# Kernel tuning notes

Measured on AMD Instinct MI355X. Metric: run time of the kernel, lower is better.

Reference implementation:

```python
import jax, jax.numpy as jnp
import numpy as np

LAYERS = 2      # LightGCN propagation layers
LAMB = 0.5      # aux loss weight
REG = 1e-4      # embedding reg weight
N_AUX = 2       # len(behaviors) - 1


def setup_inputs() -> dict:
    key = jax.random.key(0)
    k = jax.random.split(key, 8)
    n_users, n_items, d = 100000, 50000, 32
    E = 1000000
    user_emb = (jax.random.normal(k[0], (n_users + 1, d), jnp.float32) * 0.1).at[0].set(0.0)
    item_emb = (jax.random.normal(k[1], (n_items + 1, d), jnp.float32) * 0.1).at[0].set(0.0)
    aux_u = jax.random.randint(k[2], (N_AUX, E), 1, n_users + 1)
    aux_i = jax.random.randint(k[3], (N_AUX, E), 1, n_items + 1)
    aux_edges = jnp.stack([aux_u, aux_i], axis=-1).astype(jnp.int32)
    tgt_u = jax.random.randint(k[4], (E,), 1, n_users + 1)
    tgt_i = jax.random.randint(k[5], (E,), 1, n_items + 1)
    target_edges = jnp.stack([tgt_u, tgt_i], axis=-1).astype(jnp.int32)
    # [B, 1+N_AUX, 3]: per row (user, pos_item, neg_item) for target then each aux behavior
    batch_data = jax.random.randint(k[6], (4096, 1 + N_AUX, 3), 1, n_items + 1).astype(jnp.int32)
    return {"user_emb": user_emb, "item_emb": item_emb, "batch_data": batch_data,
            "aux_edges": aux_edges, "target_edges": target_edges}


def _graph(edges, n_user_rows, N):
    """Symmetric-normalized bipartite LightGCN graph as directed COO (src, dst, w)."""
    u = edges[:, 0]
    v = edges[:, 1] + n_user_rows  # shift item ids into joint node space
    ones = jnp.ones(u.shape[0], jnp.float32)
    deg = jax.ops.segment_sum(ones, u, num_segments=N) + jax.ops.segment_sum(ones, v, num_segments=N)
    dinv = jnp.where(deg > 0, jax.lax.rsqrt(jnp.maximum(deg, 1.0)), 0.0)
    w = dinv[u] * dinv[v]
    src = jnp.concatenate([u, v])
    dst = jnp.concatenate([v, u])
    w2 = jnp.concatenate([w, w])
    return src, dst, w2


def _lightgcn(emb, src, dst, w, N):
    """L-layer LightGCN propagation, mean over layers 0..L."""
    acc = emb
    cur = emb
    for _ in range(LAYERS):
        cur = jax.ops.segment_sum(w[:, None] * cur[src], dst, num_segments=N)
        acc = acc + cur
    return acc / (LAYERS + 1)


def _prob(ue, ie, u, i):
    return jax.nn.relu(jnp.sum(ue[u] * ie[i], axis=-1))


def _bpr(p, n):
    return -jnp.mean(jax.nn.log_sigmoid(p - n))


def reference(user_emb, item_emb, batch_data, aux_edges, target_edges):
    Nu = user_emb.shape[0]
    N = Nu + item_emb.shape[0]
    all_emb = jnp.concatenate([user_emb, item_emb], axis=0)
    tgt_g = _graph(target_edges, Nu, N)

    user, p_item, n_item = batch_data[:, 0, 0], batch_data[:, 0, 1], batch_data[:, 0, 2]
    aux_user, aux_p, aux_n = batch_data[:, 1:, 0], batch_data[:, 1:, 1], batch_data[:, 1:, 2]

    cps, cns, dps, dns, aps, ans, aux_losses = [], [], [], [], [], [], []
    for idx in range(N_AUX):
        # combine graph = aux behavior edges union target edges
        comb_edges = jnp.concatenate([aux_edges[idx], target_edges], axis=0)
        ce = _lightgcn(all_emb, *_graph(comb_edges, Nu, N), N)
        cu, ci = ce[:Nu], ce[Nu:]
        cps.append(_prob(cu, ci, user, p_item))
        cns.append(_prob(cu, ci, user, n_item))

        ae = _lightgcn(all_emb, *_graph(aux_edges[idx], Nu, N), N)
        au, ai = ae[:Nu], ae[Nu:]
        aps.append(_prob(au, ai, user, p_item))
        ans.append(_prob(au, ai, user, n_item))

        # condition: propagate aux embeddings through the target graph
        de = _lightgcn(ae, *tgt_g, N)
        du, di = de[:Nu], de[Nu:]
        dps.append(_prob(du, di, user, p_item))
        dns.append(_prob(du, di, user, n_item))

        ps = jnp.sum(au[aux_user[:, idx]] * ai[aux_p[:, idx]], axis=-1)
        ns = jnp.sum(au[aux_user[:, idx]] * ai[aux_n[:, idx]], axis=-1)
        aux_losses.append(_bpr(ps, ns))

    aux_loss = jnp.mean(jnp.stack(aux_losses))

    def front_door(cond, comb, aux):
        return jnp.sum(cond * jnp.sum(comb * aux, axis=0), axis=0)

    p_scores = front_door(jnp.stack(dps), jnp.stack(cps), jnp.stack(aps))
    n_scores = front_door(jnp.stack(dns), jnp.stack(cns), jnp.stack(ans))
    rec_loss = _bpr(p_scores, n_scores)
    emb_loss = (jnp.linalg.norm(user_emb) + jnp.linalg.norm(item_emb)) / item_emb.shape[0]
    return rec_loss + LAMB * aux_loss + REG * emb_loss
```

## Files before the change

kernel.cpp:

```cpp
#include <hip/hip_runtime.h>
#include <hip/hip_fp16.h>
#include <math.h>

#define D 32
#define ROWU 16
#define NBK 1024
#define BSHIFT 8
#define TILE_H 16384
#define TILE_BIN 2048

typedef unsigned int u32;
typedef unsigned short u16;

__device__ __forceinline__ float logsigf(float x) {
  return fminf(x, 0.f) - log1pf(expf(-fabsf(x)));
}

__device__ __forceinline__ float lo16(u32 u) { return __uint_as_float(u << 16); }
__device__ __forceinline__ float hi16(u32 u) { return __uint_as_float(u & 0xFFFF0000u); }
__device__ __forceinline__ u32 pk2(float a, float b) {
  u32 ua = __float_as_uint(a), ub = __float_as_uint(b);
  u32 ra = (ua + 0x7FFFu + ((ua >> 16) & 1u)) >> 16;
  u32 rb = (ub + 0x7FFFu + ((ub >> 16) & 1u)) >> 16;
  return (ra & 0xFFFFu) | (rb << 16);
}
__device__ __forceinline__ float bfat(const u16* __restrict__ p, size_t off) {
  return __uint_as_float(((u32)p[off]) << 16);
}
__device__ __forceinline__ void accum8(float* a, float w, uint4 x) {
  a[0] += w * lo16(x.x); a[1] += w * hi16(x.x);
  a[2] += w * lo16(x.y); a[3] += w * hi16(x.y);
  a[4] += w * lo16(x.z); a[5] += w * hi16(x.z);
  a[6] += w * lo16(x.w); a[7] += w * hi16(x.w);
}
__device__ __forceinline__ uint4 pack8(const float* a, float w) {
  return make_uint4(pk2(w * a[0], w * a[1]), pk2(w * a[2], w * a[3]),
                    pk2(w * a[4], w * a[5]), pk2(w * a[6], w * a[7]));
}

__device__ __forceinline__ u32 wpack(float a, float b) {
  __half2 h = __floats2half2_rn(a, b);
  return *reinterpret_cast<u32*>(&h);
}
__device__ __forceinline__ float2 hun(int wb) {
  __half2 h;
  *reinterpret_cast<int*>(&h) = wb;
  return __half22float2(h);
}


__global__ void hist_kernel(const int2* __restrict__ tgt, const int2* __restrict__ aux,
                            int E, int Nu, int BPS, int* __restrict__ bcur) {
  __shared__ int lh[NBK];
  int seg = blockIdx.x / BPS;
  int blk = blockIdx.x - seg * BPS;
  const int2* edges = (seg == 0) ? tgt : aux + (size_t)(seg - 1) * E;
  for (int b = threadIdx.x; b < NBK; b += 256) lh[b] = 0;
  __syncthreads();
  int e0 = blk * TILE_H;
  for (int k = threadIdx.x; k < TILE_H; k += 256) {
    int e = e0 + k;
    if (e < E) {
      int2 ed = edges[e];
      atomicAdd(&lh[ed.x >> BSHIFT], 1);
      atomicAdd(&lh[(ed.y + Nu) >> BSHIFT], 1);
    }
  }
  __syncthreads();
  for (int b = threadIdx.x; b < NBK; b += 256)
    if (lh[b]) atomicAdd(&bcur[seg * NBK + b], lh[b]);
}

__global__ void bscan_kernel(int* __restrict__ bcur) {
  int* b = bcur + blockIdx.x * NBK;
  int lane = threadIdx.x;
  int carry = 0;
  for (int base = 0; base < NBK; base += 64) {
    int i = base + lane;
    int v = b[i];
    int s = v;
    #pragma unroll
    for (int o = 1; o < 64; o <<= 1) {
      int t = __shfl_up(s, o);
      if (lane >= o) s += t;
    }
    b[i] = carry + s - v;
    carry += __shfl(s, 63);
  }
}

__global__ void bin_kernel(const int2* __restrict__ tgt, const int2* __restrict__ aux,
                           int E, int Nu, int BPS, int* __restrict__ bcur,
                           int* __restrict__ binned) {
  __shared__ int stage[2 * TILE_BIN];
  __shared__ u16 stagebk[2 * TILE_BIN];
  __shared__ int lh[NBK];
  __shared__ int loff[NBK];
  __shared__ int gb[NBK];
  __shared__ int wred[4];
  __shared__ int stot;
  int seg = blockIdx.x / BPS;
  int blk = blockIdx.x - seg * BPS;
  const int2* edges = (seg == 0) ? tgt : aux + (size_t)(seg - 1) * E;
  int* out = binned + (size_t)seg * 2 * E;
  int tid = threadIdx.x;
  for (int b = tid; b < NBK; b += 256) lh[b] = 0;
  __syncthreads();
  int e0 = blk * TILE_BIN;
  int pkv[16];
  int pb[16];
  int pr[16];
  #pragma unroll
  for (int it = 0; it < 8; ++it) {
    int e = e0 + tid + it * 256;
    bool ok = e < E;
    int2 ed = ok ? edges[e] : make_int2(0, -Nu);
    int u = ed.x, v = ed.y + Nu;
    int b1 = u >> BSHIFT, b2 = v >> BSHIFT;
    pkv[2 * it] = ((u & 255) << 18) | v;
    pb[2 * it] = b1;
    pr[2 * it] = ok ? atomicAdd(&lh[b1], 1) : 0;
    pkv[2 * it + 1] = ((v & 255) << 18) | u;
    pb[2 * it + 1] = b2;
    pr[2 * it + 1] = ok ? atomicAdd(&lh[b2], 1) : 0;
  }
  __syncthreads();
  int lane = tid & 63, wid = tid >> 6;
  int b4 = tid * 4;
  int v0 = lh[b4], v1 = lh[b4 + 1], v2 = lh[b4 + 2], v3 = lh[b4 + 3];
  int tsum = v0 + v1 + v2 + v3;
  int incl = tsum;
  #pragma unroll
  for (int o = 1; o < 64; o <<= 1) {
    int t = __shfl_up(incl, o);
    if (lane >= o) incl += t;
  }
  if (lane == 63) wred[wid] = incl;
  __syncthreads();
  int wbase = 0;
  for (int w = 0; w < wid; ++w) wbase += wred[w];
  int excl = wbase + incl - tsum;
  loff[b4] = excl;
  loff[b4 + 1] = excl + v0;
  loff[b4 + 2] = excl + v0 + v1;
  loff[b4 + 3] = excl + v0 + v1 + v2;
  if (tid == 255) stot = excl + tsum;
  #pragma unroll
  for (int j = 0; j < 4; ++j) {
    int b = b4 + j;
    int c = lh[b];
    gb[b] = c ? atomicAdd(&bcur[seg * NBK + b], c) : 0;
  }
  __syncthreads();
  #pragma unroll
  for (int it = 0; it < 16; ++it) {
    int e = e0 + tid + (it >> 1) * 256;
    if (e < E) {
      int pos = loff[pb[it]] + pr[it];
      stage[pos] = pkv[it];
      stagebk[pos] = (u16)pb[it];
    }
  }
  __syncthreads();
  int tot = stot;
  for (int k = tid; k < tot; k += 256) {
    int b = stagebk[k];
    out[gb[b] + (k - loff[b])] = stage[k];
  }
}

__global__ void csr_count_kernel(const int* __restrict__ binned,
                                 const int* __restrict__ bend, int E2, int N, int NBKe,
                                 int* __restrict__ deg3, int* __restrict__ rp3) {
  __shared__ int cnt[256];
  __shared__ int wred[4];
  int seg = blockIdx.x / NBKe;
  int bkt = blockIdx.x - seg * NBKe;
  int node0 = bkt << BSHIFT;
  const int* bc = bend + seg * NBK;
  int start = (bkt == 0) ? 0 : bc[bkt - 1];
  int end = bc[bkt];
  int cntE = end - start;
  const int* src = binned + (size_t)seg * E2 + start;
  cnt[threadIdx.x] = 0;
  __syncthreads();
  for (int k = threadIdx.x; k < cntE; k += 256) atomicAdd(&cnt[src[k] >> 18], 1);
  __syncthreads();
  int lane = threadIdx.x & 63, wid = threadIdx.x >> 6;
  int v = cnt[threadIdx.x];
  int incl = v;
  #pragma unroll
  for (int o = 1; o < 64; o <<= 1) {
    int t = __shfl_up(incl, o);
    if (lane >= o) incl += t;
  }
  if (lane == 63) wred[wid] = incl;
  __syncthreads();
  int wbase = 0;
  for (int w = 0; w < wid; ++w) wbase += wred[w];
  int node = node0 + (int)threadIdx.x;
  if (node < N) {
    deg3[(size_t)seg * N + node] = v;
    rp3[(size_t)seg * (N + 1) + node] = start + wbase + incl - v;
  }
  if (bkt == 0 && threadIdx.x == 0) rp3[(size_t)seg * (N + 1) + N] = E2;
}

__global__ void dinv_all_kernel(const int* __restrict__ deg3, float* __restrict__ dinv5,
                                u32* __restrict__ wtab, int N) {
  int n = blockIdx.x * blockDim.x + threadIdx.x;
  if (n >= N) return;
  int dt = deg3[n], d0 = deg3[N + n], d1 = deg3[2 * N + n];
  float wt  = dt ? rsqrtf((float)dt) : 0.f;
  float wa0 = d0 ? rsqrtf((float)d0) : 0.f;
  float wa1 = d1 ? rsqrtf((float)d1) : 0.f;
  int c0 = dt + d0, c1 = dt + d1;
  float wc0 = c0 ? rsqrtf((float)c0) : 0.f;
  float wc1 = c1 ? rsqrtf((float)c1) : 0.f;
  dinv5[n] = wt;
  dinv5[N + n] = wa0;
  dinv5[2 * N + n] = wa1;
  dinv5[3 * N + n] = wc0;
  dinv5[4 * N + n] = wc1;
  wtab[n] = wpack(wc0, wc1);
  wtab[N + n] = wpack(wa0, wc0);
  wtab[2 * N + n] = wpack(wa1, wc1);
}

__global__ void csr_scatter_kernel(const int* __restrict__ binned,
                                   const int* __restrict__ bend,
                                   const int* __restrict__ rp3,
                                   const u32* __restrict__ wtab,
                                   int E2, int N, int NBKe,
                                   int2* __restrict__ pk) {
  __shared__ int cnt[256];
  __shared__ int off[256];
  int seg = blockIdx.x / NBKe;
  int bkt = blockIdx.x - seg * NBKe;
  int node0 = bkt << BSHIFT;
  const int* bc = bend + seg * NBK;
  int start = (bkt == 0) ? 0 : bc[bkt - 1];
  int end = bc[bkt];
  int cntE = end - start;
  const int* src = binned + (size_t)seg * E2 + start;
  int node = node0 + (int)threadIdx.x;
  off[threadIdx.x] = (node < N) ? rp3[(size_t)seg * (N + 1) + node] : 0;
  cnt[threadIdx.x] = 0;
  const u32* wt = wtab + (size_t)seg * N;
  __syncthreads();
  int2* out = pk + (size_t)seg * E2;
  for (int k = threadIdx.x; k < cntE; k += 256) {
    int en = src[k];
    int lb = en >> 18;
    int c = en & 0x3FFFF;
    int pos = atomicAdd(&cnt[lb], 1);
    out[off[lb] + pos] = make_int2(c, (int)wt[c]);
  }
}

__global__ void cvt_emb_kernel(const float2* __restrict__ ue, long nu2,
                               const float2* __restrict__ ie, long ni2,
                               u32* __restrict__ emb) {
  long i = (long)blockIdx.x * blockDim.x + threadIdx.x;
  if (i >= nu2 + ni2) return;
  float2 v = (i < nu2) ? ue[i] : ie[i - nu2];
  emb[i] = pk2(v.x, v.y);
}


__device__ __forceinline__ void edge1_dual(const int2* __restrict__ p, int j, int lane,
                                           const uint4* __restrict__ rows,
                                           float* a1, float* a2) {
  int2 en = p[j];
  float2 w = hun(en.y);
  uint4 x = rows[(size_t)en.x * 4 + lane];
  accum8(a1, w.x, x);
  accum8(a2, w.y, x);
}

__device__ __forceinline__ void stream_dual(const int* __restrict__ rp,
                                            const int2* __restrict__ p, int n, int lane,
                                            const uint4* __restrict__ rows,
                                            float* a1, float* a2) {
  int j = rp[n], e = rp[n + 1];
  if ((j & 1) && j < e) { edge1_dual(p, j, lane, rows, a1, a2); ++j; }
  for (; j + 3 < e; j += 4) {
    int4 m0 = *reinterpret_cast<const int4*>(p + j);
    int4 m1 = *reinterpret_cast<const int4*>(p + j + 2);
    uint4 x0 = rows[(size_t)m0.x * 4 + lane];
    uint4 x1 = rows[(size_t)m0.z * 4 + lane];
    uint4 x2 = rows[(size_t)m1.x * 4 + lane];
    uint4 x3 = rows[(size_t)m1.z * 4 + lane];
    float2 w0 = hun(m0.y), w1 = hun(m0.w), w2 = hun(m1.y), w3 = hun(m1.w);
    accum8(a1, w0.x, x0); accum8(a2, w0.y, x0);
    accum8(a1, w1.x, x1); accum8(a2, w1.y, x1);
    accum8(a1, w2.x, x2); accum8(a2, w2.y, x2);
    accum8(a1, w3.x, x3); accum8(a2, w3.y, x3);
  }
  for (; j < e; ++j) edge1_dual(p, j, lane, rows, a1, a2);
}

__global__ void gather_fused_all_kernel(const int* __restrict__ rp3,
                                        const int2* __restrict__ pk,
                                        const float* __restrict__ dinv5,
                                        const uint4* __restrict__ emb,
                                        uint4* __restrict__ BaAll, uint4* __restrict__ BcAll,
                                        int N, int E2) {
  const int* rpA0 = rp3 + (size_t)(N + 1);
  const int* rpA1 = rp3 + 2 * (size_t)(N + 1);
  const int2* pT = pk;
  const int2* pA0 = pk + (size_t)E2;
  const int2* pA1 = pk + 2 * (size_t)E2;
  const float* dvA0 = dinv5 + (size_t)N;
  const float* dvA1 = dinv5 + 2 * (size_t)N;
  const float* dvC0 = dinv5 + 3 * (size_t)N;
  const float* dvC1 = dinv5 + 4 * (size_t)N;
  int t = blockIdx.x * blockDim.x + threadIdx.x;
  int n = t >> 2;
  if (n >= N) return;
  int lane = t & 3;
  float aA0[8] = {0, 0, 0, 0, 0, 0, 0, 0};
  float aA1[8] = {0, 0, 0, 0, 0, 0, 0, 0};
  float aC0[8] = {0, 0, 0, 0, 0, 0, 0, 0};
  float aC1[8] = {0, 0, 0, 0, 0, 0, 0, 0};
  stream_dual(rpA0, pA0, n, lane, emb, aA0, aC0);
  stream_dual(rpA1, pA1, n, lane, emb, aA1, aC1);
  stream_dual(rp3, pT, n, lane, emb, aC0, aC1);
  size_t o = (size_t)n * 4 + lane;
  size_t rowN4 = (size_t)N * 4;
  BaAll[o] = pack8(aA0, dvA0[n]);
  BaAll[rowN4 + o] = pack8(aA1, dvA1[n]);
  BcAll[o] = pack8(aC0, dvC0[n]);
  BcAll[rowN4 + o] = pack8(aC1, dvC1[n]);
}

__global__ void gather_avg_kernel(const int* __restrict__ rp3, const int2* __restrict__ pk,
                                  const float* __restrict__ dinv5,
                                  const uint4* __restrict__ emb,
                                  const uint4* __restrict__ BaAll, uint4* __restrict__ AI,
                                  int N, int E2) {
  int idx = blockIdx.y;
  const int* rp = rp3 + (size_t)(1 + idx) * (N + 1);
  const int2* pA = pk + (size_t)(1 + idx) * E2;
  const float* dv = dinv5 + (size_t)(1 + idx) * N;
  const uint4* cur = BaAll + (size_t)idx * N * 4;
  int t = blockIdx.x * blockDim.x + threadIdx.x;
  int n = t >> 2;
  if (n >= N) return;
  int lane = t & 3;
  float acc[8] = {0, 0, 0, 0, 0, 0, 0, 0};
  int j = rp[n], e = rp[n + 1];
  if ((j & 1) && j < e) {
    int2 en = pA[j];
    uint4 x = cur[(size_t)en.x * 4 + lane];
    accum8(acc, hun(en.y).x, x);
    ++j;
  }
  for (; j + 3 < e; j += 4) {
    int4 m0 = *reinterpret_cast<const int4*>(pA + j);
    int4 m1 = *reinterpret_cast<const int4*>(pA + j + 2);
    uint4 x0 = cur[(size_t)m0.x * 4 + lane];
    uint4 x1 = cur[(size_t)m0.z * 4 + lane];
    uint4 x2 = cur[(size_t)m1.x * 4 + lane];
    uint4 x3 = cur[(size_t)m1.z * 4 + lane];
    accum8(acc, hun(m0.y).x, x0);
    accum8(acc, hun(m0.w).x, x1);
    accum8(acc, hun(m1.y).x, x2);
    accum8(acc, hun(m1.w).x, x3);
  }
  for (; j < e; ++j) {
    int2 en = pA[j];
    uint4 x = cur[(size_t)en.x * 4 + lane];
    accum8(acc, hun(en.y).x, x);
  }
  float wn = dv[n];
  uint4 e4 = emb[(size_t)n * 4 + lane];
  uint4 b4 = cur[(size_t)n * 4 + lane];
  float r[8];
  r[0] = (lo16(e4.x) + lo16(b4.x) + wn * acc[0]) * (1.f / 3.f);
  r[1] = (hi16(e4.x) + hi16(b4.x) + wn * acc[1]) * (1.f / 3.f);
  r[2] = (lo16(e4.y) + lo16(b4.y) + wn * acc[2]) * (1.f / 3.f);
  r[3] = (hi16(e4.y) + hi16(b4.y) + wn * acc[3]) * (1.f / 3.f);
  r[4] = (lo16(e4.z) + lo16(b4.z) + wn * acc[4]) * (1.f / 3.f);
  r[5] = (hi16(e4.z) + hi16(b4.z) + wn * acc[5]) * (1.f / 3.f);
  r[6] = (lo16(e4.w) + lo16(b4.w) + wn * acc[6]) * (1.f / 3.f);
  r[7] = (hi16(e4.w) + hi16(b4.w) + wn * acc[7]) * (1.f / 3.f);
  AI[(size_t)n * 8 + idx * 4 + lane] = pack8(r, 1.f);
}

__global__ void de_gather_kernel(const int* __restrict__ rp3, const int2* __restrict__ pk,
                                 const float* __restrict__ dinv5,
                                 const uint4* __restrict__ AI, uint4* __restrict__ DeI,
                                 int N) {
  int t = blockIdx.x * blockDim.x + threadIdx.x;
  int n = t >> 3;
  if (n >= N) return;
  int lane = t & 7;
  float acc[8] = {0, 0, 0, 0, 0, 0, 0, 0};
  int j = rp3[n], e = rp3[n + 1];
  if ((j & 1) && j < e) {
    int c = pk[j].x;
    uint4 x = AI[(size_t)c * 8 + lane];
    accum8(acc, dinv5[c], x);
    ++j;
  }
  for (; j + 3 < e; j += 4) {
    int4 m0 = *reinterpret_cast<const int4*>(pk + j);
    int4 m1 = *reinterpret_cast<const int4*>(pk + j + 2);
    uint4 x0 = AI[(size_t)m0.x * 8 + lane];
    uint4 x1 = AI[(size_t)m0.z * 8 + lane];
    uint4 x2 = AI[(size_t)m1.x * 8 + lane];
    uint4 x3 = AI[(size_t)m1.z * 8 + lane];
    accum8(acc, dinv5[m0.x], x0);
    accum8(acc, dinv5[m0.z], x1);
    accum8(acc, dinv5[m1.x], x2);
    accum8(acc, dinv5[m1.z], x3);
  }
  for (; j < e; ++j) {
    int c = pk[j].x;
    uint4 x = AI[(size_t)c * 8 + lane];
    accum8(acc, dinv5[c], x);
  }
  DeI[(size_t)n * 8 + lane] = pack8(acc, dinv5[n]);
}


__device__ __forceinline__ float fdim2(const int2* __restrict__ pkA, const int2* __restrict__ pkT,
                                       const int* __restrict__ rpA, const int* __restrict__ rpT,
                                       int idx, const float* __restrict__ dv,
                                       const u16* __restrict__ base, const u16* __restrict__ L1,
                                       int r, int d) {
  float acc = 0.f;
  for (int j = rpA[r]; j < rpA[r + 1]; ++j) {
    int2 en = pkA[j];
    acc += hun(en.y).y * bfat(L1, (size_t)en.x * D + d);
  }
  for (int j = rpT[r]; j < rpT[r + 1]; ++j) {
    int2 en = pkT[j];
    float2 w = hun(en.y);
    acc += (idx ? w.y : w.x) * bfat(L1, (size_t)en.x * D + d);
  }
  return (bfat(base, (size_t)r * D + d) + bfat(L1, (size_t)r * D + d) + dv[r] * acc) * (1.f / 3.f);
}

__device__ __forceinline__ float fdim1i(const int2* __restrict__ pkT, const int* __restrict__ rp,
                                        const float* __restrict__ dv,
                                        const u16* __restrict__ base, const u16* __restrict__ L1,
                                        int r, int di) {
  float acc = 0.f;
  for (int j = rp[r]; j < rp[r + 1]; ++j) {
    int2 en = pkT[j];
    acc += dv[en.x] * bfat(L1, (size_t)en.x * 64 + di);
  }
  return (bfat(base, (size_t)r * 64 + di) + bfat(L1, (size_t)r * 64 + di) + dv[r] * acc) * (1.f / 3.f);
}

__global__ void ce_sparse_kernel(const int* __restrict__ rp3, const int2* __restrict__ pk,
                                 const float* __restrict__ dinv5,
                                 const u32* __restrict__ EMBu, const u32* __restrict__ BcAll,
                                 const int* __restrict__ batch, int Bsz, int Nu, int N, int E2,
                                 float* __restrict__ cps, float* __restrict__ cns) {
  int idx = blockIdx.y;
  const int* rpA = rp3 + (size_t)(1 + idx) * (N + 1);
  const int2* pkA = pk + (size_t)(1 + idx) * E2;
  const float* dv = dinv5 + (size_t)(3 + idx) * N;
  const u16* base = (const u16*)EMBu;
  const u16* L1 = (const u16*)(BcAll + (size_t)idx * N * ROWU);
  float* outp = cps + (size_t)idx * Bsz;
  float* outn = cns + (size_t)idx * Bsz;
  int t = blockIdx.x * blockDim.x + threadIdx.x;
  int b = t >> 5, d = t & 31;
  if (b >= Bsz) return;
  int u = batch[b * 9 + 0];
  int p = batch[b * 9 + 1] + Nu;
  int n = batch[b * 9 + 2] + Nu;
  float uv = fdim2(pkA, pk, rpA, rp3, idx, dv, base, L1, u, d);
  float pv = fdim2(pkA, pk, rpA, rp3, idx, dv, base, L1, p, d);
  float nv = fdim2(pkA, pk, rpA, rp3, idx, dv, base, L1, n, d);
  float sp = uv * pv, sn = uv * nv;
  #pragma unroll
  for (int o = 16; o > 0; o >>= 1) {
    sp += __shfl_down(sp, o, 32);
    sn += __shfl_down(sn, o, 32);
  }
  if (d == 0) {
    outp[b] = fmaxf(sp, 0.f);
    outn[b] = fmaxf(sn, 0.f);
  }
}

__global__ void de_sparse_kernel(const int* __restrict__ rp3, const int2* __restrict__ pk,
                                 const float* __restrict__ dinv5,
                                 const u32* __restrict__ AI, const u32* __restrict__ DeI,
                                 const int* __restrict__ batch, int Bsz, int Nu, int N,
                                 float* __restrict__ dps, float* __restrict__ dns) {
  int idx = blockIdx.y;
  const u16* base = (const u16*)AI;
  const u16* L1 = (const u16*)DeI;
  float* outp = dps + (size_t)idx * Bsz;
  float* outn = dns + (size_t)idx * Bsz;
  int t = blockIdx.x * blockDim.x + threadIdx.x;
  int b = t >> 5, d = t & 31;
  if (b >= Bsz) return;
  int di = idx * 32 + d;
  int u = batch[b * 9 + 0];
  int p = batch[b * 9 + 1] + Nu;
  int n = batch[b * 9 + 2] + Nu;
  float uv = fdim1i(pk, rp3, dinv5, base, L1, u, di);
  float pv = fdim1i(pk, rp3, dinv5, base, L1, p, di);
  float nv = fdim1i(pk, rp3, dinv5, base, L1, n, di);
  float sp = uv * pv, sn = uv * nv;
  #pragma unroll
  for (int o = 16; o > 0; o >>= 1) {
    sp += __shfl_down(sp, o, 32);
    sn += __shfl_down(sn, o, 32);
  }
  if (d == 0) {
    outp[b] = fmaxf(sp, 0.f);
    outn[b] = fmaxf(sn, 0.f);
  }
}


__device__ __forceinline__ float dotrow(const u32* __restrict__ a, const u32* __restrict__ b) {
  float s = 0.f;
  #pragma unroll
  for (int k = 0; k < ROWU; ++k) {
    u32 x = a[k], y = b[k];
    s += lo16(x) * lo16(y) + hi16(x) * hi16(y);
  }
  return s;
}

__global__ void score_aux_kernel(const u32* __restrict__ AI, const int* __restrict__ batch,
                                 int Bsz, int Nu, int N, float* __restrict__ aps,
                                 float* __restrict__ ans_, float* __restrict__ accs) {
  int idx = blockIdx.y;
  const u32* A = AI + (size_t)idx * ROWU;
  float* outp = aps + (size_t)idx * Bsz;
  float* outn = ans_ + (size_t)idx * Bsz;
  int b = blockIdx.x * blockDim.x + threadIdx.x;
  float l = 0.f;
  if (b < Bsz) {
    int u = batch[b * 9 + 0];
    int p = batch[b * 9 + 1] + Nu;
    int n = batch[b * 9 + 2] + Nu;
    const u32* ur = A + (size_t)u * 32;
    outp[b] = fmaxf(dotrow(ur, A + (size_t)p * 32), 0.f);
    outn[b] = fmaxf(dotrow(ur, A + (size_t)n * 32), 0.f);
    const int* r = batch + b * 9 + 3 * (1 + idx);
    const u32* aur = A + (size_t)r[0] * 32;
    float ps = dotrow(aur, A + (size_t)(r[1] + Nu) * 32);
    float ns = dotrow(aur, A + (size_t)(r[2] + Nu) * 32);
    l = -logsigf(ps - ns);
  }
  for (int o = 32; o > 0; o >>= 1) l += __shfl_down(l, o);
  if ((threadIdx.x & 63) == 0) atomicAdd(&accs[idx], l);
}

__global__ void recloss_kernel(const float* __restrict__ cps, const float* __restrict__ cns,
                               const float* __restrict__ aps, const float* __restrict__ ans_,
                               const float* __restrict__ dps, const float* __restrict__ dns,
                               int Bsz, int NA, float* __restrict__ acc) {
  int b = blockIdx.x * blockDim.x + threadIdx.x;
  float l = 0.f;
  if (b < Bsz) {
    float dp = 0.f, dn = 0.f, cap = 0.f, can = 0.f;
    for (int i = 0; i < NA; ++i) {
      dp += dps[i * Bsz + b];
      dn += dns[i * Bsz + b];
      cap += cps[i * Bsz + b] * aps[i * Bsz + b];
      can += cns[i * Bsz + b] * ans_[i * Bsz + b];
    }
    l = -logsigf(dp * cap - dn * can);
  }
  for (int o = 32; o > 0; o >>= 1) l += __shfl_down(l, o);
  if ((threadIdx.x & 63) == 0) atomicAdd(acc, l);
}

__global__ void sumsq2_kernel(const float4* __restrict__ xu, int n4u,
                              const float4* __restrict__ xi, int n4i,
                              float* __restrict__ accU, float* __restrict__ accI) {
  __shared__ float redU[4], redI[4];
  int tid = threadIdx.x;
  int gid = blockIdx.x * blockDim.x + tid;
  int stride = gridDim.x * blockDim.x;
  float su = 0.f, si = 0.f;
  for (int i = gid; i < n4u; i += stride) {
    float4 v = xu[i];
    su += v.x * v.x + v.y * v.y + v.z * v.z + v.w * v.w;
  }
  for (int i = gid; i < n4i; i += stride) {
    float4 v = xi[i];
    si += v.x * v.x + v.y * v.y + v.z * v.z + v.w * v.w;
  }
  for (int o = 32; o > 0; o >>= 1) {
    su += __shfl_down(su, o);
    si += __shfl_down(si, o);
  }
  if ((tid & 63) == 0) { redU[tid >> 6] = su; redI[tid >> 6] = si; }
  __syncthreads();
  if (tid == 0) {
    atomicAdd(accU, redU[0] + redU[1] + redU[2] + redU[3]);
    atomicAdd(accI, redI[0] + redI[1] + redI[2] + redI[3]);
  }
}

__global__ void final_kernel(const float* __restrict__ accs, int Bsz, int NA, int NiRows,
                             float* __restrict__ out) {
  float rec = accs[NA] / (float)Bsz;
  float aux = 0.f;
  for (int i = 0; i < NA; ++i) aux += accs[i] / (float)Bsz;
  aux /= (float)NA;
  float embl = (sqrtf(accs[NA + 1]) + sqrtf(accs[NA + 2])) / (float)NiRows;
  out[0] = rec + 0.5f * aux + 1e-4f * embl;
}

extern "C" void kernel_launch(void* const* d_in, const int* in_sizes, int n_in,
                              void* d_out, int out_size, void* d_ws, size_t ws_size,
                              hipStream_t stream) {
  const float* user_emb = (const float*)d_in[0];
  const float* item_emb = (const float*)d_in[1];
  const int* batch = (const int*)d_in[2];
  const int* aux_edges = (const int*)d_in[3];
  const int* tgt_edges = (const int*)d_in[4];

  const int NuRows = in_sizes[0] / D;
  const int NiRows = in_sizes[1] / D;
  const int Bsz = in_sizes[2] / 9;
  const int E = in_sizes[4] / 2;
  const int NA = in_sizes[3] / (2 * E);
  const int N = NuRows + NiRows;
  const int E2 = 2 * E;
  const size_t rowH = (size_t)N * ROWU;
  const int BPS_H = (E + TILE_H - 1) / TILE_H;
  const int BPS_B = (E + TILE_BIN - 1) / TILE_BIN;
  const int NBKe = (N + (1 << BSHIFT) - 1) >> BSHIFT;

  u32* EMBu = (u32*)d_ws;
  u32* AI = EMBu + rowH;
  u32* BaAll = AI + 2 * rowH;
  u32* BcAll = BaAll + 2 * rowH;
  int* deg3 = (int*)(BcAll + 2 * rowH);
  float* dinv5 = (float*)(deg3 + 3 * (size_t)N);
  u32* wtab = (u32*)(dinv5 + 5 * (size_t)N);
  int* rp3 = (int*)(wtab + 3 * (size_t)N);
  int* bcur = rp3 + 3 * (size_t)(N + 1);
  uintptr_t pka = ((uintptr_t)(bcur + 3 * (size_t)NBK) + 15) & ~(uintptr_t)15;
  int2* pk = (int2*)pka;
  float* cps = (float*)(pk + 3 * (size_t)E2);
  float* cns = cps + (size_t)NA * Bsz;
  float* aps = cns + (size_t)NA * Bsz;
  float* ans_ = aps + (size_t)NA * Bsz;
  float* dps = ans_ + (size_t)NA * Bsz;
  float* dns = dps + (size_t)NA * Bsz;
  float* accs = dns + (size_t)NA * Bsz;
  int* binned = (int*)AI;

  const int TB = 256;
  const int gN = (N + TB - 1) / TB;
  const int gN4 = (N * 4 + TB - 1) / TB;
  const int gN8 = (N * 8 + TB - 1) / TB;
  const int gB = (Bsz + TB - 1) / TB;
  const int gB32 = (Bsz * 32 + TB - 1) / TB;
  const long nu2 = (long)NuRows * ROWU;
  const long ni2 = (long)NiRows * ROWU;
  const int gCvt = (int)((nu2 + ni2 + TB - 1) / TB);

  cvt_emb_kernel<<<gCvt, TB, 0, stream>>>((const float2*)user_emb, nu2,
                                          (const float2*)item_emb, ni2, EMBu);

  hipMemsetAsync(bcur, 0, 3 * (size_t)NBK * sizeof(int), stream);
  hist_kernel<<<3 * BPS_H, TB, 0, stream>>>((const int2*)tgt_edges, (const int2*)aux_edges,
                                            E, NuRows, BPS_H, bcur);
  bscan_kernel<<<3, 64, 0, stream>>>(bcur);
  bin_kernel<<<3 * BPS_B, TB, 0, stream>>>((const int2*)tgt_edges, (const int2*)aux_edges,
                                           E, NuRows, BPS_B, bcur, binned);
  csr_count_kernel<<<3 * NBKe, TB, 0, stream>>>(binned, bcur, E2, N, NBKe, deg3, rp3);
  dinv_all_kernel<<<gN, TB, 0, stream>>>(deg3, dinv5, wtab, N);
  csr_scatter_kernel<<<3 * NBKe, TB, 0, stream>>>(binned, bcur, rp3, wtab, E2, N, NBKe, pk);

  hipMemsetAsync(accs, 0, (size_t)(NA + 3) * sizeof(float), stream);

  dim3 gridG(gN4, NA), gridB(gB, NA), gridS(gB32, NA);

  gather_fused_all_kernel<<<gN4, TB, 0, stream>>>(rp3, pk, dinv5, (const uint4*)EMBu,
                                                  (uint4*)BaAll, (uint4*)BcAll, N, E2);
  gather_avg_kernel<<<gridG, TB, 0, stream>>>(rp3, pk, dinv5, (const uint4*)EMBu,
                                              (const uint4*)BaAll, (uint4*)AI, N, E2);
  score_aux_kernel<<<gridB, TB, 0, stream>>>(AI, batch, Bsz, NuRows, N, aps, ans_, accs);
  ce_sparse_kernel<<<gridS, TB, 0, stream>>>(rp3, pk, dinv5, EMBu, BcAll,
                                             batch, Bsz, NuRows, N, E2, cps, cns);
  de_gather_kernel<<<gN8, TB, 0, stream>>>(rp3, pk, dinv5, (const uint4*)AI,
                                           (uint4*)BaAll, N);
  de_sparse_kernel<<<gridS, TB, 0, stream>>>(rp3, pk, dinv5, AI, (const u32*)BaAll,
                                             batch, Bsz, NuRows, N, dps, dns);

  sumsq2_kernel<<<104, TB, 0, stream>>>((const float4*)user_emb,
                                        (int)((size_t)NuRows * D / 4),
                                        (const float4*)item_emb,
                                        (int)((size_t)NiRows * D / 4),
                                        accs + NA + 1, accs + NA + 2);
  recloss_kernel<<<gB, TB, 0, stream>>>(cps, cns, aps, ans_, dps, dns, Bsz, NA, accs + NA);
  final_kernel<<<1, 1, 0, stream>>>(accs, Bsz, NA, NiRows, (float*)d_out);
}
```

Before: 641.6 us.

## Replace bucketed binning CSR build with global atomic degree count and scatter

Replaces the two-pass bucket-binning CSR construction (shared-memory histograms, staged bin writes, per-bucket count and scatter) with a direct global-atomic degree histogram, a three-phase prefix scan, and a per-edge atomic cursor scatter into the CSR. This removes the intermediate binned array and several shared-memory staging passes. In exchange it relies on about 6M global atomics spread over random nodes and scattered 8-byte writes with poor locality. Neighbor order within each row also becomes nondeterministic, which can change floating-point summation order.

```diff
diff --git a/kernel.cpp b/kernel.cpp
--- a/kernel.cpp
+++ b/kernel.cpp
@@ -4,10 +4,6 @@
 
 #define D 32
 #define ROWU 16
-#define NBK 1024
-#define BSHIFT 8
-#define TILE_H 16384
-#define TILE_BIN 2048
 
 typedef unsigned int u32;
 typedef unsigned short u16;
@@ -49,161 +45,92 @@
 }
 
 
-__global__ void hist_kernel(const int2* __restrict__ tgt, const int2* __restrict__ aux,
-                            int E, int Nu, int BPS, int* __restrict__ bcur) {
-  __shared__ int lh[NBK];
-  int seg = blockIdx.x / BPS;
-  int blk = blockIdx.x - seg * BPS;
+__global__ void deg_hist_kernel(const int2* __restrict__ tgt, const int2* __restrict__ aux,
+                                int E, int Nu, int N, int* __restrict__ deg3) {
+  int e = blockIdx.x * blockDim.x + threadIdx.x;
+  if (e >= E) return;
+  int seg = blockIdx.y;
   const int2* edges = (seg == 0) ? tgt : aux + (size_t)(seg - 1) * E;
-  for (int b = threadIdx.x; b < NBK; b += 256) lh[b] = 0;
+  int2 ed = edges[e];
+  int* dg = deg3 + (size_t)seg * N;
+  atomicAdd(&dg[ed.x], 1);
+  atomicAdd(&dg[ed.y + Nu], 1);
+}
+
+__global__ void scanA_kernel(const int* __restrict__ deg3, int* __restrict__ rp3,
+                             int* __restrict__ pbs, int N) {
+  __shared__ int wred[4];
+  int seg = blockIdx.y;
+  int n0 = blockIdx.x * 1024 + threadIdx.x * 4;
+  const int* dg = deg3 + (size_t)seg * N;
+  int v0 = 0, v1 = 0, v2 = 0, v3 = 0;
+  if (n0 < N) {
+    v0 = dg[n0];
+    if (n0 + 1 < N) v1 = dg[n0 + 1];
+    if (n0 + 2 < N) v2 = dg[n0 + 2];
+    if (n0 + 3 < N) v3 = dg[n0 + 3];
+  }
+  int tsum = v0 + v1 + v2 + v3;
+  int lane = threadIdx.x & 63, wid = threadIdx.x >> 6;
+  int incl = tsum;
+  #pragma unroll
+  for (int o = 1; o < 64; o <<= 1) {
+    int t = __shfl_up(incl, o);
+    if (lane >= o) incl += t;
+  }
+  if (lane == 63) wred[wid] = incl;
   __syncthreads();
-  int e0 = blk * TILE_H;
-  for (int k = threadIdx.x; k < TILE_H; k += 256) {
-    int e = e0 + k;
-    if (e < E) {
-      int2 ed = edges[e];
-      atomicAdd(&lh[ed.x >> BSHIFT], 1);
-      atomicAdd(&lh[(ed.y + Nu) >> BSHIFT], 1);
-    }
-  }
-  __syncthreads();
-  for (int b = threadIdx.x; b < NBK; b += 256)
-    if (lh[b]) atomicAdd(&bcur[seg * NBK + b], lh[b]);
-}
-
-__global__ void bscan_kernel(int* __restrict__ bcur) {
-  int* b = bcur + blockIdx.x * NBK;
+  int wbase = 0;
+  for (int w = 0; w < wid; ++w) wbase += wred[w];
+  int excl = wbase + incl - tsum;
+  int* rp = rp3 + (size_t)seg * (N + 1);
+  if (n0 < N) {
+    rp[n0] = excl;
+    if (n0 + 1 < N) rp[n0 + 1] = excl + v0;
+    if (n0 + 2 < N) rp[n0 + 2] = excl + v0 + v1;
+    if (n0 + 3 < N) rp[n0 + 3] = excl + v0 + v1 + v2;
+  }
+  if (threadIdx.x == 255)
+    pbs[seg * 256 + blockIdx.x] = wbase + incl;
+}
+
+__global__ void scanB_kernel(int* __restrict__ pbs, int nb) {
+  int* b = pbs + blockIdx.x * 256;
   int lane = threadIdx.x;
   int carry = 0;
-  for (int base = 0; base < NBK; base += 64) {
+  for (int base = 0; base < nb; base += 64) {
     int i = base + lane;
-    int v = b[i];
+    int v = (i < nb) ? b[i] : 0;
     int s = v;
     #pragma unroll
     for (int o = 1; o < 64; o <<= 1) {
       int t = __shfl_up(s, o);
       if (lane >= o) s += t;
     }
-    b[i] = carry + s - v;
+    if (i < nb) b[i] = carry + s - v;
     carry += __shfl(s, 63);
   }
 }
 
-__global__ void bin_kernel(const int2* __restrict__ tgt, const int2* __restrict__ aux,
-                           int E, int Nu, int BPS, int* __restrict__ bcur,
-                           int* __restrict__ binned) {
-  __shared__ int stage[2 * TILE_BIN];
-  __shared__ u16 stagebk[2 * TILE_BIN];
-  __shared__ int lh[NBK];
-  __shared__ int loff[NBK];
-  __shared__ int gb[NBK];
-  __shared__ int wred[4];
-  __shared__ int stot;
-  int seg = blockIdx.x / BPS;
-  int blk = blockIdx.x - seg * BPS;
-  const int2* edges = (seg == 0) ? tgt : aux + (size_t)(seg - 1) * E;
-  int* out = binned + (size_t)seg * 2 * E;
-  int tid = threadIdx.x;
-  for (int b = tid; b < NBK; b += 256) lh[b] = 0;
-  __syncthreads();
-  int e0 = blk * TILE_BIN;
-  int pkv[16];
-  int pb[16];
-  int pr[16];
-  #pragma unroll
-  for (int it = 0; it < 8; ++it) {
-    int e = e0 + tid + it * 256;
-    bool ok = e < E;
-    int2 ed = ok ? edges[e] : make_int2(0, -Nu);
-    int u = ed.x, v = ed.y + Nu;
-    int b1 = u >> BSHIFT, b2 = v >> BSHIFT;
-    pkv[2 * it] = ((u & 255) << 18) | v;
-    pb[2 * it] = b1;
-    pr[2 * it] = ok ? atomicAdd(&lh[b1], 1) : 0;
-    pkv[2 * it + 1] = ((v & 255) << 18) | u;
-    pb[2 * it + 1] = b2;
-    pr[2 * it + 1] = ok ? atomicAdd(&lh[b2], 1) : 0;
-  }
-  __syncthreads();
-  int lane = tid & 63, wid = tid >> 6;
-  int b4 = tid * 4;
-  int v0 = lh[b4], v1 = lh[b4 + 1], v2 = lh[b4 + 2], v3 = lh[b4 + 3];
-  int tsum = v0 + v1 + v2 + v3;
-  int incl = tsum;
-  #pragma unroll
-  for (int o = 1; o < 64; o <<= 1) {
-    int t = __shfl_up(incl, o);
-    if (lane >= o) incl += t;
-  }
-  if (lane == 63) wred[wid] = incl;
-  __syncthreads();
-  int wbase = 0;
-  for (int w = 0; w < wid; ++w) wbase += wred[w];
-  int excl = wbase + incl - tsum;
-  loff[b4] = excl;
-  loff[b4 + 1] = excl + v0;
-  loff[b4 + 2] = excl + v0 + v1;
-  loff[b4 + 3] = excl + v0 + v1 + v2;
-  if (tid == 255) stot = excl + tsum;
-  #pragma unroll
-  for (int j = 0; j < 4; ++j) {
-    int b = b4 + j;
-    int c = lh[b];
-    gb[b] = c ? atomicAdd(&bcur[seg * NBK + b], c) : 0;
-  }
-  __syncthreads();
-  #pragma unroll
-  for (int it = 0; it < 16; ++it) {
-    int e = e0 + tid + (it >> 1) * 256;
-    if (e < E) {
-      int pos = loff[pb[it]] + pr[it];
-      stage[pos] = pkv[it];
-      stagebk[pos] = (u16)pb[it];
+__global__ void scanC_kernel(int* __restrict__ rp3, int* __restrict__ cur3,
+                             const int* __restrict__ pbs, int N, int E2) {
+  int seg = blockIdx.y;
+  int n0 = blockIdx.x * 1024 + threadIdx.x * 4;
+  int off = pbs[seg * 256 + blockIdx.x];
+  int* rp = rp3 + (size_t)seg * (N + 1);
+  int* cur = cur3 + (size_t)seg * N;
+  if (n0 < N) {
+    #pragma unroll
+    for (int k = 0; k < 4; ++k) {
+      int n = n0 + k;
+      if (n < N) {
+        int v = rp[n] + off;
+        rp[n] = v;
+        cur[n] = v;
+      }
     }
   }
-  __syncthreads();
-  int tot = stot;
-  for (int k = tid; k < tot; k += 256) {
-    int b = stagebk[k];
-    out[gb[b] + (k - loff[b])] = stage[k];
-  }
-}
-
-__global__ void csr_count_kernel(const int* __restrict__ binned,
-                                 const int* __restrict__ bend, int E2, int N, int NBKe,
-                                 int* __restrict__ deg3, int* __restrict__ rp3) {
-  __shared__ int cnt[256];
-  __shared__ int wred[4];
-  int seg = blockIdx.x / NBKe;
-  int bkt = blockIdx.x - seg * NBKe;
-  int node0 = bkt << BSHIFT;
-  const int* bc = bend + seg * NBK;
-  int start = (bkt == 0) ? 0 : bc[bkt - 1];
-  int end = bc[bkt];
-  int cntE = end - start;
-  const int* src = binned + (size_t)seg * E2 + start;
-  cnt[threadIdx.x] = 0;
-  __syncthreads();
-  for (int k = threadIdx.x; k < cntE; k += 256) atomicAdd(&cnt[src[k] >> 18], 1);
-  __syncthreads();
-  int lane = threadIdx.x & 63, wid = threadIdx.x >> 6;
-  int v = cnt[threadIdx.x];
-  int incl = v;
-  #pragma unroll
-  for (int o = 1; o < 64; o <<= 1) {
-    int t = __shfl_up(incl, o);
-    if (lane >= o) incl += t;
-  }
-  if (lane == 63) wred[wid] = incl;
-  __syncthreads();
-  int wbase = 0;
-  for (int w = 0; w < wid; ++w) wbase += wred[w];
-  int node = node0 + (int)threadIdx.x;
-  if (node < N) {
-    deg3[(size_t)seg * N + node] = v;
-    rp3[(size_t)seg * (N + 1) + node] = start + wbase + incl - v;
-  }
-  if (bkt == 0 && threadIdx.x == 0) rp3[(size_t)seg * (N + 1) + N] = E2;
+  if (blockIdx.x == 0 && threadIdx.x == 0) rp[N] = E2;
 }
 
 __global__ void dinv_all_kernel(const int* __restrict__ deg3, float* __restrict__ dinv5,
@@ -227,35 +154,24 @@
   wtab[2 * N + n] = wpack(wa1, wc1);
 }
 
-__global__ void csr_scatter_kernel(const int* __restrict__ binned,
-                                   const int* __restrict__ bend,
-                                   const int* __restrict__ rp3,
-                                   const u32* __restrict__ wtab,
-                                   int E2, int N, int NBKe,
-                                   int2* __restrict__ pk) {
-  __shared__ int cnt[256];
-  __shared__ int off[256];
-  int seg = blockIdx.x / NBKe;
-  int bkt = blockIdx.x - seg * NBKe;
-  int node0 = bkt << BSHIFT;
-  const int* bc = bend + seg * NBK;
-  int start = (bkt == 0) ? 0 : bc[bkt - 1];
-  int end = bc[bkt];
-  int cntE = end - start;
-  const int* src = binned + (size_t)seg * E2 + start;
-  int node = node0 + (int)threadIdx.x;
-  off[threadIdx.x] = (node < N) ? rp3[(size_t)seg * (N + 1) + node] : 0;
-  cnt[threadIdx.x] = 0;
+__global__ void pk_scatter_kernel(const int2* __restrict__ tgt, const int2* __restrict__ aux,
+                                  int E, int Nu, int N, int E2,
+                                  const u32* __restrict__ wtab, int* __restrict__ cur3,
+                                  int2* __restrict__ pk) {
+  int e = blockIdx.x * blockDim.x + threadIdx.x;
+  if (e >= E) return;
+  int seg = blockIdx.y;
+  const int2* edges = (seg == 0) ? tgt : aux + (size_t)(seg - 1) * E;
+  int2 ed = edges[e];
+  int u = ed.x, v = ed.y + Nu;
   const u32* wt = wtab + (size_t)seg * N;
-  __syncthreads();
+  int* cur = cur3 + (size_t)seg * N;
   int2* out = pk + (size_t)seg * E2;
-  for (int k = threadIdx.x; k < cntE; k += 256) {
-    int en = src[k];
-    int lb = en >> 18;
-    int c = en & 0x3FFFF;
-    int pos = atomicAdd(&cnt[lb], 1);
-    out[off[lb] + pos] = make_int2(c, (int)wt[c]);
-  }
+  u32 wu = wt[u], wv = wt[v];
+  int pu = atomicAdd(&cur[u], 1);
+  out[pu] = make_int2(v, (int)wv);
+  int pv = atomicAdd(&cur[v], 1);
+  out[pv] = make_int2(u, (int)wu);
 }
 
 __global__ void cvt_emb_kernel(const float2* __restrict__ ue, long nu2,
@@ -633,20 +549,15 @@
   const int N = NuRows + NiRows;
   const int E2 = 2 * E;
   const size_t rowH = (size_t)N * ROWU;
-  const int BPS_H = (E + TILE_H - 1) / TILE_H;
-  const int BPS_B = (E + TILE_BIN - 1) / TILE_BIN;
-  const int NBKe = (N + (1 << BSHIFT) - 1) >> BSHIFT;
 
   u32* EMBu = (u32*)d_ws;
   u32* AI = EMBu + rowH;
   u32* BaAll = AI + 2 * rowH;
   u32* BcAll = BaAll + 2 * rowH;
-  int* deg3 = (int*)(BcAll + 2 * rowH);
-  float* dinv5 = (float*)(deg3 + 3 * (size_t)N);
+  float* dinv5 = (float*)(BcAll + 2 * rowH);
   u32* wtab = (u32*)(dinv5 + 5 * (size_t)N);
   int* rp3 = (int*)(wtab + 3 * (size_t)N);
-  int* bcur = rp3 + 3 * (size_t)(N + 1);
-  uintptr_t pka = ((uintptr_t)(bcur + 3 * (size_t)NBK) + 15) & ~(uintptr_t)15;
+  uintptr_t pka = ((uintptr_t)(rp3 + 3 * (size_t)(N + 1)) + 15) & ~(uintptr_t)15;
   int2* pk = (int2*)pka;
   float* cps = (float*)(pk + 3 * (size_t)E2);
   float* cns = cps + (size_t)NA * Bsz;
@@ -655,7 +566,9 @@
   float* dps = ans_ + (size_t)NA * Bsz;
   float* dns = dps + (size_t)NA * Bsz;
   float* accs = dns + (size_t)NA * Bsz;
-  int* binned = (int*)AI;
+  int* deg3 = (int*)AI;
+  int* cur3 = (int*)BaAll;
+  int* pbs = cur3 + 3 * (size_t)N;
 
   const int TB = 256;
   const int gN = (N + TB - 1) / TB;
@@ -663,6 +576,8 @@
   const int gN8 = (N * 8 + TB - 1) / TB;
   const int gB = (Bsz + TB - 1) / TB;
   const int gB32 = (Bsz * 32 + TB - 1) / TB;
+  const int gE = (E + TB - 1) / TB;
+  const int nb = (N + 1023) / 1024;
   const long nu2 = (long)NuRows * ROWU;
   const long ni2 = (long)NiRows * ROWU;
   const int gCvt = (int)((nu2 + ni2 + TB - 1) / TB);
@@ -670,15 +585,16 @@
   cvt_emb_kernel<<<gCvt, TB, 0, stream>>>((const float2*)user_emb, nu2,
                                           (const float2*)item_emb, ni2, EMBu);
 
-  hipMemsetAsync(bcur, 0, 3 * (size_t)NBK * sizeof(int), stream);
-  hist_kernel<<<3 * BPS_H, TB, 0, stream>>>((const int2*)tgt_edges, (const int2*)aux_edges,
-                                            E, NuRows, BPS_H, bcur);
-  bscan_kernel<<<3, 64, 0, stream>>>(bcur);
-  bin_kernel<<<3 * BPS_B, TB, 0, stream>>>((const int2*)tgt_edges, (const int2*)aux_edges,
-                                           E, NuRows, BPS_B, bcur, binned);
-  csr_count_kernel<<<3 * NBKe, TB, 0, stream>>>(binned, bcur, E2, N, NBKe, deg3, rp3);
+  hipMemsetAsync(deg3, 0, 3 * (size_t)N * sizeof(int), stream);
+  dim3 gridE(gE, 3), gridSc(nb, 3);
+  deg_hist_kernel<<<gridE, TB, 0, stream>>>((const int2*)tgt_edges, (const int2*)aux_edges,
+                                            E, NuRows, N, deg3);
+  scanA_kernel<<<gridSc, TB, 0, stream>>>(deg3, rp3, pbs, N);
+  scanB_kernel<<<3, 64, 0, stream>>>(pbs, nb);
   dinv_all_kernel<<<gN, TB, 0, stream>>>(deg3, dinv5, wtab, N);
-  csr_scatter_kernel<<<3 * NBKe, TB, 0, stream>>>(binned, bcur, rp3, wtab, E2, N, NBKe, pk);
+  scanC_kernel<<<gridSc, TB, 0, stream>>>(rp3, cur3, pbs, N, E2);
+  pk_scatter_kernel<<<gridE, TB, 0, stream>>>((const int2*)tgt_edges, (const int2*)aux_edges,
+                                              E, NuRows, N, E2, wtab, cur3, pk);
 
   hipMemsetAsync(accs, 0, (size_t)(NA + 3) * sizeof(float), stream);
 
```

Measured after the change: 1.084 ms. 1.69x slower.
